# Optimization experiments

Measured on AMD Instinct MI355X. Metric: run time of the kernel, lower is better.

Reference implementation:

```python
import jax, jax.numpy as jnp
import numpy as np

N_STORE, N_DEPT, F_IN = 100_000, 20_000, 128
E = 1_000_000
H, C = 4, 16  # heads, per-head channels; hidden = H*C = 64
NUM_LAYERS = 3


def setup_inputs() -> dict:
    key = jax.random.key(0)
    ks = jax.random.split(key, 16)
    def edges(k, n_src, n_dst):
        k1, k2 = jax.random.split(k)
        src = jax.random.randint(k1, (E,), 0, n_src, dtype=jnp.int32)
        dst = jax.random.randint(k2, (E,), 0, n_dst, dtype=jnp.int32)
        return jnp.stack([src, dst])
    s = 0.05
    return {
        "x_store": jax.random.normal(ks[0], (N_STORE, F_IN), jnp.float32),
        "x_dept": jax.random.normal(ks[1], (N_DEPT, F_IN), jnp.float32),
        "edge_sd": edges(ks[2], N_STORE, N_DEPT),   # store -> dept
        "edge_ds": edges(ks[3], N_DEPT, N_STORE),   # dept  -> store
        "edge_ss": edges(ks[4], N_STORE, N_STORE),  # store -> store
        "W_src0": jax.random.normal(ks[5], (3, F_IN, H * C), jnp.float32) * s,
        "W_dst0": jax.random.normal(ks[6], (3, F_IN, H * C), jnp.float32) * s,
        "W_src_h": jax.random.normal(ks[7], (2, 3, H * C, H * C), jnp.float32) * s,
        "W_dst_h": jax.random.normal(ks[8], (2, 3, H * C, H * C), jnp.float32) * s,
        "att_src": jax.random.normal(ks[9], (3, 3, H, C), jnp.float32) * s,
        "att_dst": jax.random.normal(ks[10], (3, 3, H, C), jnp.float32) * s,
        "bias": jnp.zeros((3, 3, H * C), jnp.float32),
    }


def gat_conv(x_src, x_dst, edge, W_s, W_d, a_s, a_d, b, n_dst):
    """PyG GATConv, bipartite, add_self_loops=False, eval mode (no dropout)."""
    h_s = (x_src @ W_s).reshape(-1, H, C)   # [N_src, H, C]
    h_d = (x_dst @ W_d).reshape(-1, H, C)   # [N_dst, H, C]
    al_s = jnp.sum(h_s * a_s, axis=-1)      # [N_src, H]
    al_d = jnp.sum(h_d * a_d, axis=-1)      # [N_dst, H]
    src, dst = edge[0], edge[1]
    e = jax.nn.leaky_relu(al_s[src] + al_d[dst], 0.2)        # [E, H]
    m = jax.ops.segment_max(e, dst, num_segments=n_dst)       # segment softmax
    m = jnp.where(jnp.isfinite(m), m, 0.0)
    ex = jnp.exp(e - m[dst])
    denom = jax.ops.segment_sum(ex, dst, num_segments=n_dst)
    alpha = ex / (denom[dst] + 1e-16)                          # [E, H]
    msg = h_s[src] * alpha[:, :, None]                         # [E, H, C]
    out = jax.ops.segment_sum(msg, dst, num_segments=n_dst)    # [N_dst, H, C]
    return out.reshape(n_dst, H * C) + b


def _forward(x_store, x_dept, edge_sd, edge_ds, edge_ss,
             W_src0, W_dst0, W_src_h, W_dst_h, att_src, att_dst, bias):
    xs, xd = x_store, x_dept
    for i in range(NUM_LAYERS):
        Ws = W_src0 if i == 0 else W_src_h[i - 1]
        Wd = W_dst0 if i == 0 else W_dst_h[i - 1]
        # edge type 0: store->dept ; 1: dept->store ; 2: store->store
        o_dept = gat_conv(xs, xd, edge_sd, Ws[0], Wd[0], att_src[i, 0], att_dst[i, 0], bias[i, 0], N_DEPT)
        o1 = gat_conv(xd, xs, edge_ds, Ws[1], Wd[1], att_src[i, 1], att_dst[i, 1], bias[i, 1], N_STORE)
        o2 = gat_conv(xs, xs, edge_ss, Ws[2], Wd[2], att_src[i, 2], att_dst[i, 2], bias[i, 2], N_STORE)
        o_store = (o1 + o2) * 0.5  # HeteroConv aggr='mean' across relations into 'store'
        if i < NUM_LAYERS - 1:
            xs, xd = jax.nn.relu(o_store), jax.nn.relu(o_dept)  # dropout is identity in eval
        else:
            xs, xd = o_store, o_dept
    return jnp.concatenate([xs, xd], axis=0)  # [N_STORE + N_DEPT, 64]


def reference(x_store, x_dept, edge_sd, edge_ds, edge_ss,
              W_src0, W_dst0, W_src_h, W_dst_h, att_src, att_dst, bias):
    return _forward(x_store, x_dept, edge_sd, edge_ds, edge_ss,
                    W_src0, W_dst0, W_src_h, W_dst_h, att_src, att_dst, bias)
```

## Files before the change

### kernel.cpp

```cpp
#include <hip/hip_runtime.h>
#include <hip/hip_bf16.h>

#define N_STORE 100000
#define N_DEPT  20000
#define F_IN    128
#define NTOT    (N_DEPT + 2 * N_STORE)

#define NB0   157
#define NB12  196
#define NBUCK (NB0 + 2 * NB12)

using u16    = unsigned short;
using bf16x8 = __attribute__((ext_vector_type(8))) __bf16;
using f32x4  = __attribute__((ext_vector_type(4))) float;

__device__ __forceinline__ float b2f(u16 x) {
    unsigned u = ((unsigned)x) << 16;
    return __builtin_bit_cast(float, u);
}
__device__ __forceinline__ u16 f2b(float f) {
    unsigned u = __builtin_bit_cast(unsigned, f);
    u += 0x7FFFu + ((u >> 16) & 1u);
    return (u16)(u >> 16);
}

__global__ void k_zeroi(int* p, int n) {
    int i = blockIdx.x * 256 + threadIdx.x;
    if (i < n) p[i] = 0;
}

__global__ void k_bcount(const int* __restrict__ e0, const int* __restrict__ e1,
                         const int* __restrict__ e2, int E, int* __restrict__ bucketCnt) {
    __shared__ int c[256];
    int t = threadIdx.x;
    c[t] = 0; __syncthreads();
    int rel = blockIdx.y;
    const int* e = (rel == 0) ? e0 : (rel == 1) ? e1 : e2;
    int n = (rel == 0) ? N_DEPT : N_STORE;
    int shift = (rel == 0) ? 7 : 9;
    int i0 = blockIdx.x * 2048 + t;
#pragma unroll
    for (int k = 0; k < 8; ++k) {
        int i = i0 + k * 256;
        if (i < E) {
            int d = e[E + i];
            if ((unsigned)d < (unsigned)n) atomicAdd(&c[d >> shift], 1);
        }
    }
    __syncthreads();
    int bbase = (rel == 0) ? 0 : (rel == 1) ? NB0 : NB0 + NB12;
    int nb = (rel == 0) ? NB0 : NB12;
    if (t < nb && c[t]) atomicAdd(&bucketCnt[bbase + t], c[t]);
}

__global__ void k_bscan(const int* __restrict__ bucketCnt, int* __restrict__ bucketOfs,
                        int* __restrict__ bucketCur, int* __restrict__ offs) {
    __shared__ int s[1024];
    int t = threadIdx.x;
    int v = (t < NBUCK) ? bucketCnt[t] : 0;
    s[t] = v; __syncthreads();
    for (int o = 1; o < 1024; o <<= 1) {
        int u = (t >= o) ? s[t - o] : 0;
        __syncthreads();
        s[t] += u;
        __syncthreads();
    }
    if (t < NBUCK) {
        bucketOfs[t + 1] = s[t];
        bucketCur[t] = s[t] - v;
    }
    if (t == 0) bucketOfs[0] = 0;
    if (t == NBUCK - 1) offs[NTOT] = s[t];
}

__global__ void k_bscatter(const int* __restrict__ e0, const int* __restrict__ e1,
                           const int* __restrict__ e2, int E,
                           int* __restrict__ bucketCur, unsigned* __restrict__ pairs) {
    __shared__ int c[256];
    __shared__ int base[256];
    int t = threadIdx.x;
    c[t] = 0; __syncthreads();
    int rel = blockIdx.y;
    const int* e = (rel == 0) ? e0 : (rel == 1) ? e1 : e2;
    int n = (rel == 0) ? N_DEPT : N_STORE;
    int shift = (rel == 0) ? 7 : 9;
    int i0 = blockIdx.x * 2048 + t;
    int mb[8], mr[8]; unsigned mv[8];
#pragma unroll
    for (int k = 0; k < 8; ++k) {
        int i = i0 + k * 256;
        mb[k] = -1;
        if (i < E) {
            int d = e[E + i];
            if ((unsigned)d < (unsigned)n) {
                int b = d >> shift;
                mb[k] = b;
                mr[k] = atomicAdd(&c[b], 1);
                mv[k] = (unsigned)e[i] | ((unsigned)(d - (b << shift)) << 20);
            }
        }
    }
    __syncthreads();
    int bbase = (rel == 0) ? 0 : (rel == 1) ? NB0 : NB0 + NB12;
    int nb = (rel == 0) ? NB0 : NB12;
    if (t < nb && c[t]) base[t] = atomicAdd(&bucketCur[bbase + t], c[t]);
    __syncthreads();
#pragma unroll
    for (int k = 0; k < 8; ++k)
        if (mb[k] >= 0) pairs[base[mb[k]] + mr[k]] = mv[k];
}

__global__ void k_bfinal(const unsigned* __restrict__ pairs, const int* __restrict__ bucketOfs,
                         int* __restrict__ offs, int* __restrict__ srcs_all) {
    int b = blockIdx.x, t = threadIdx.x;
    int rel = (b < NB0) ? 0 : (b < NB0 + NB12) ? 1 : 2;
    int shift = (rel == 0) ? 7 : 9;
    int bLocal = b - ((rel == 0) ? 0 : (rel == 1) ? NB0 : NB0 + NB12);
    int n = (rel == 0) ? N_DEPT : N_STORE;
    int gbase = (rel == 0) ? 0 : (rel == 1) ? N_DEPT : N_DEPT + N_STORE;
    int nodeLo = bLocal << shift;
    int bsize = 1 << shift;
    int nNodes = n - nodeLo; if (nNodes > bsize) nNodes = bsize;
    int pairLo = bucketOfs[b], pairHi = bucketOfs[b + 1];
    __shared__ int cnt[512], sc[512];
    cnt[t] = 0; cnt[t + 256] = 0;
    __syncthreads();
    for (int p = pairLo + t; p < pairHi; p += 256)
        atomicAdd(&cnt[pairs[p] >> 20], 1);
    __syncthreads();
    sc[t] = cnt[t]; sc[t + 256] = cnt[t + 256];
    __syncthreads();
    for (int o = 1; o < 512; o <<= 1) {
        int a0 = (t >= o) ? sc[t - o] : 0;
        int a1 = (t + 256 >= o) ? sc[t + 256 - o] : 0;
        __syncthreads();
        sc[t] += a0; sc[t + 256] += a1;
        __syncthreads();
    }
    int ex0 = sc[t] - cnt[t];
    int ex1 = sc[t + 256] - cnt[t + 256];
    if (t < nNodes)       offs[gbase + nodeLo + t]       = pairLo + ex0;
    if (t + 256 < nNodes) offs[gbase + nodeLo + t + 256] = pairLo + ex1;
    __syncthreads();
    cnt[t] = ex0; cnt[t + 256] = ex1;
    __syncthreads();
    for (int p = pairLo + t; p < pairHi; p += 256) {
        unsigned u = pairs[p];
        int q = atomicAdd(&cnt[u >> 20], 1);
        srcs_all[pairLo + q] = (int)(u & 0xFFFFFu);
    }
}

__global__ void k_pack_store(const float* __restrict__ Wa, const float* __restrict__ Wb,
                             const float* __restrict__ Wd1, const float* __restrict__ Wd2,
                             const float* __restrict__ aS0, const float* __restrict__ aS2,
                             const float* __restrict__ aD1, const float* __restrict__ aD2,
                             int K, u16* __restrict__ out) {
    int id = blockIdx.x * 256 + threadIdx.x;
    int total = K * 144;
    if (id >= total) return;
    int k = id / 144, n = id - k * 144;
    float val;
    if (n < 64) val = Wa[k * 64 + n];
    else if (n < 128) val = Wb[k * 64 + (n - 64)];
    else {
        int g = (n - 128) >> 2, h = (n - 128) & 3;
        const float* W = (g == 0) ? Wa : (g == 1) ? Wb : (g == 2) ? Wd1 : Wd2;
        const float* a = (g == 0) ? aS0 : (g == 1) ? aS2 : (g == 2) ? aD1 : aD2;
        float acc = 0.f;
        for (int c = 0; c < 16; ++c) acc += W[k * 64 + h * 16 + c] * a[h * 16 + c];
        val = acc;
    }
    int KT = K >> 5;
    int ct = n >> 4, col = n & 15, kt = k >> 5, q = (k >> 3) & 3, j = k & 7;
    out[(size_t)((ct * KT + kt) * 64 + q * 16 + col) * 8 + j] = f2b(val);
}

__global__ void k_pack_dept(const float* __restrict__ Ws1, const float* __restrict__ Wd0,
                            const float* __restrict__ aD0, const float* __restrict__ aS1,
                            int K, u16* __restrict__ out) {
    int id = blockIdx.x * 256 + threadIdx.x;
    int total = K * 80;
    if (id >= total) return;
    int k = id / 80, n = id - k * 80;
    float val;
    if (n < 64) val = Ws1[k * 64 + n];
    else if (n < 72) {
        int g = (n - 64) >> 2, h = (n - 64) & 3;
        const float* W = g ? Ws1 : Wd0;
        const float* a = g ? aS1 : aD0;
        float acc = 0.f;
        for (int c = 0; c < 16; ++c) acc += W[k * 64 + h * 16 + c] * a[h * 16 + c];
        val = acc;
    } else val = 0.f;
    int KT = K >> 5;
    int ct = n >> 4, col = n & 15, kt = k >> 5, q = (k >> 3) & 3, j = k & 7;
    out[(size_t)((ct * KT + kt) * 64 + q * 16 + col) * 8 + j] = f2b(val);
}

template <int KT, int CVT>
__global__ void k_gemm(const void* __restrict__ Ain, int nrows, int K,
                       const u16* __restrict__ Bpanel, int CT,
                       u16* __restrict__ C, int cstride) {
    int wid = (blockIdx.x * blockDim.x + threadIdx.x) >> 6;
    int lane = threadIdx.x & 63;
    int m0 = wid << 4;
    if (m0 >= nrows) return;
    int r = lane & 15, q = lane >> 4;
    bf16x8 a[KT];
    if (CVT) {
        const float* ap = (const float*)Ain + (size_t)(m0 + r) * K + q * 8;
#pragma unroll
        for (int kt = 0; kt < KT; ++kt) {
            f32x4 f0 = *(const f32x4*)(ap + kt * 32);
            f32x4 f1 = *(const f32x4*)(ap + kt * 32 + 4);
            bf16x8 v;
#pragma unroll
            for (int j = 0; j < 4; ++j) {
                v[j]     = __builtin_bit_cast(__bf16, f2b(f0[j]));
                v[4 + j] = __builtin_bit_cast(__bf16, f2b(f1[j]));
            }
            a[kt] = v;
        }
    } else {
        const u16* ap = (const u16*)Ain + (size_t)(m0 + r) * K + q * 8;
#pragma unroll
        for (int kt = 0; kt < KT; ++kt) a[kt] = *(const bf16x8*)(ap + kt * 32);
    }
    const bf16x8* B = (const bf16x8*)Bpanel;
    for (int ct = 0; ct < CT; ++ct) {
        f32x4 acc = {0.f, 0.f, 0.f, 0.f};
#pragma unroll
        for (int kt = 0; kt < KT; ++kt)
            acc = __builtin_amdgcn_mfma_f32_16x16x32_bf16(a[kt], B[(ct * KT + kt) * 64 + lane], acc, 0, 0, 0);
        u16* cp = C + (size_t)m0 * cstride + ct * 16 + r;
#pragma unroll
        for (int i = 0; i < 4; ++i) cp[(size_t)(q * 4 + i) * cstride] = f2b(acc[i]);
    }
}

__device__ __forceinline__ float warp16_sum(float v) {
    v += __shfl_xor(v, 1);
    v += __shfl_xor(v, 2);
    v += __shfl_xor(v, 4);
    v += __shfl_xor(v, 8);
    return v;
}

template <int UB>
__device__ __forceinline__ void agg_seg(const int* __restrict__ srcs, int j0, int j1, int nsrc,
                                        const u16* __restrict__ tab, int stride, int hsOff, int alsOff,
                                        int lane, int slot, int h, int pbase, float ald,
                                        float& acc, float& den) {
    for (int j = j0; j < j1; j += 16) {
        int nb = j1 - j; if (nb > 16) nb = 16;
        int sv = srcs[j + (slot < nb ? slot : 0)];
        sv = ((unsigned)sv < (unsigned)nsrc) ? sv : 0;
        float av = b2f(tab[(size_t)sv * stride + alsOff + h]);
        float e = av + ald;
        e = (e > 0.f) ? e : 0.2f * e;
        float ex = (slot < nb) ? __expf(e) : 0.f;
        den += ex;
        int exi = __builtin_bit_cast(int, ex);
        for (int jj = 0; jj < nb; ) {
            int m = nb - jj; if (m > UB) m = UB;
            float exk[UB], hvk[UB];
#pragma unroll
            for (int k = 0; k < UB; ++k) {
                int idx = jj + (k < m ? k : 0);
                int s = __builtin_amdgcn_readlane(sv, idx);
                exk[k] = __builtin_bit_cast(float,
                         __builtin_amdgcn_ds_bpermute(pbase + (idx << 2), exi));
                hvk[k] = b2f(tab[(size_t)s * stride + hsOff + lane]);
            }
#pragma unroll
            for (int k = 0; k < UB; ++k)
                if (k < m) acc = fmaf(exk[k], hvk[k], acc);
            jj += m;
        }
    }
}

__global__ void k_agg1(const int* __restrict__ offs, const int* __restrict__ srcs, int ndst,
                       int nsrcmax,
                       const u16* __restrict__ srcTab, int sstride, int hsOff, int alsOff,
                       const u16* __restrict__ dstTab, int dstride, int aldOff,
                       const float* __restrict__ bias, int doRelu,
                       u16* __restrict__ bOut, float* __restrict__ fOut) {
    int wid = (blockIdx.x * blockDim.x + threadIdx.x) >> 6;
    if (wid >= ndst) return;
    int lane = threadIdx.x & 63, slot = lane & 15, h = lane >> 4;
    int pbase = (lane & 48) << 2;
    float ald = b2f(dstTab[(size_t)wid * dstride + aldOff + h]);
    int j0 = __builtin_amdgcn_readfirstlane(offs[wid]);
    int j1 = __builtin_amdgcn_readfirstlane(offs[wid + 1]);
    float acc = 0.f, den = 0.f;
    agg_seg<8>(srcs, j0, j1, nsrcmax, srcTab, sstride, hsOff, alsOff,
               lane, slot, h, pbase, ald, acc, den);
    den = warp16_sum(den);
    float out = acc / (den + 1e-16f) + bias[lane];
    if (doRelu) out = out > 0.f ? out : 0.f;
    size_t oi = (size_t)wid * 64 + lane;
    if (fOut) fOut[oi] = out;
    else      bOut[oi] = f2b(out);
}

__global__ void k_agg2(const int* __restrict__ offs1, const int* __restrict__ srcs,
                       const int* __restrict__ offs2,
                       const u16* __restrict__ projD, const u16* __restrict__ projS,
                       const float* __restrict__ bias1, const float* __restrict__ bias2,
                       int doRelu,
                       u16* __restrict__ bOut, float* __restrict__ fOut) {
    int wid = (blockIdx.x * blockDim.x + threadIdx.x) >> 6;
    if (wid >= N_STORE) return;
    int lane = threadIdx.x & 63, slot = lane & 15, h = lane >> 4;
    int pbase = (lane & 48) << 2;
    const u16* myrow = projS + (size_t)wid * 144;
    float ald1 = b2f(myrow[136 + h]);
    float ald2 = b2f(myrow[140 + h]);
    int a0 = __builtin_amdgcn_readfirstlane(offs1[wid]);
    int a1e = __builtin_amdgcn_readfirstlane(offs1[wid + 1]);
    int b0 = __builtin_amdgcn_readfirstlane(offs2[wid]);
    int b1e = __builtin_amdgcn_readfirstlane(offs2[wid + 1]);
    float acc1 = 0.f, den1 = 0.f, acc2 = 0.f, den2 = 0.f;
    agg_seg<8>(srcs, a0, a1e, N_DEPT, projD, 80, 0, 68,
               lane, slot, h, pbase, ald1, acc1, den1);
    agg_seg<8>(srcs, b0, b1e, N_STORE, projS, 144, 64, 132,
               lane, slot, h, pbase, ald2, acc2, den2);
    den1 = warp16_sum(den1);
    den2 = warp16_sum(den2);
    float out = (acc1 / (den1 + 1e-16f) + bias1[lane] + acc2 / (den2 + 1e-16f) + bias2[lane]) * 0.5f;
    if (doRelu) out = out > 0.f ? out : 0.f;
    size_t oi = (size_t)wid * 64 + lane;
    if (fOut) fOut[oi] = out;
    else      bOut[oi] = f2b(out);
}

extern "C" void kernel_launch(void* const* d_in, const int* in_sizes, int n_in,
                              void* d_out, int out_size, void* d_ws, size_t ws_size,
                              hipStream_t stream) {
    const float* x_store = (const float*)d_in[0];
    const float* x_dept  = (const float*)d_in[1];
    const int* e_sd = (const int*)d_in[2];
    const int* e_ds = (const int*)d_in[3];
    const int* e_ss = (const int*)d_in[4];
    const float* W_src0  = (const float*)d_in[5];
    const float* W_dst0  = (const float*)d_in[6];
    const float* W_src_h = (const float*)d_in[7];
    const float* W_dst_h = (const float*)d_in[8];
    const float* att_src = (const float*)d_in[9];
    const float* att_dst = (const float*)d_in[10];
    const float* bias    = (const float*)d_in[11];
    const int E = in_sizes[2] / 2;

    char* w = (char*)d_ws;
    auto alloc = [&](size_t bytes) -> char* {
        char* p = w;
        w += (bytes + 255) & ~(size_t)255;
        return p;
    };
    int* offs_all  = (int*)alloc((size_t)(NTOT + 1) * 4);
    int* srcs_all  = (int*)alloc((size_t)3 * E * 4);
    int* bucketCnt = (int*)alloc(1024 * 4);
    int* bucketOfs = (int*)alloc(1024 * 4);
    int* bucketCur = (int*)alloc(1024 * 4);
    u16* panelS[3]; u16* panelD[3];
    for (int l = 0; l < 3; ++l) {
        int KT = (l == 0) ? 4 : 2;
        panelS[l] = (u16*)alloc((size_t)KT * 9 * 64 * 8 * 2);
        panelD[l] = (u16*)alloc((size_t)KT * 5 * 64 * 8 * 2);
    }
    u16* projS  = (u16*)alloc((size_t)N_STORE * 144 * 2);
    u16* projD  = (u16*)alloc((size_t)N_DEPT * 80 * 2);
    u16* actSA  = (u16*)alloc((size_t)N_STORE * 64 * 2);
    u16* actDA  = (u16*)alloc((size_t)N_DEPT * 64 * 2);
    u16* actSB  = actSA;
    u16* actDB  = actDA;
    unsigned* pairs = (unsigned*)projS;

    int* off_sd = offs_all;
    int* off_ds = offs_all + N_DEPT;
    int* off_ss = offs_all + N_DEPT + N_STORE;

    float* outStoreF = (float*)d_out;
    float* outDeptF  = outStoreF + (size_t)N_STORE * 64;

    int ebl8 = (E + 2047) / 2048;
    k_zeroi<<<(NBUCK + 255) / 256, 256, 0, stream>>>(bucketCnt, NBUCK);
    k_bcount<<<dim3(ebl8, 3), 256, 0, stream>>>(e_sd, e_ds, e_ss, E, bucketCnt);
    k_bscan<<<1, 1024, 0, stream>>>(bucketCnt, bucketOfs, bucketCur, offs_all);
    k_bscatter<<<dim3(ebl8, 3), 256, 0, stream>>>(e_sd, e_ds, e_ss, E, bucketCur, pairs);
    k_bfinal<<<NBUCK, 256, 0, stream>>>(pairs, bucketOfs, offs_all, srcs_all);

    for (int l = 0; l < 3; ++l) {
        int K = (l == 0) ? 128 : 64;
        const float *Ws[3], *Wd[3], *aS[3], *aD[3];
        for (int rr = 0; rr < 3; ++rr) {
            Ws[rr] = (l == 0) ? W_src0 + (size_t)rr * 128 * 64
                              : W_src_h + (size_t)((l - 1) * 3 + rr) * 64 * 64;
            Wd[rr] = (l == 0) ? W_dst0 + (size_t)rr * 128 * 64
                              : W_dst_h + (size_t)((l - 1) * 3 + rr) * 64 * 64;
            aS[rr] = att_src + (size_t)(l * 3 + rr) * 64;
            aD[rr] = att_dst + (size_t)(l * 3 + rr) * 64;
        }
        k_pack_store<<<(K * 144 + 255) / 256, 256, 0, stream>>>(
            Ws[0], Ws[2], Wd[1], Wd[2], aS[0], aS[2], aD[1], aD[2], K, panelS[l]);
        k_pack_dept<<<(K * 80 + 255) / 256, 256, 0, stream>>>(
            Ws[1], Wd[0], aD[0], aS[1], K, panelD[l]);

        int gbS = (N_STORE / 16 * 64 + 255) / 256;
        int gbD = (N_DEPT / 16 * 64 + 255) / 256;
        if (l == 0) {
            k_gemm<4, 1><<<gbS, 256, 0, stream>>>(x_store, N_STORE, K, panelS[l], 9, projS, 144);
            k_gemm<4, 1><<<gbD, 256, 0, stream>>>(x_dept, N_DEPT, K, panelD[l], 5, projD, 80);
        } else if (l == 1) {
            k_gemm<2, 0><<<gbS, 256, 0, stream>>>(actSA, N_STORE, K, panelS[l], 9, projS, 144);
            k_gemm<2, 0><<<gbD, 256, 0, stream>>>(actDA, N_DEPT, K, panelD[l], 5, projD, 80);
        } else {
            k_gemm<2, 0><<<gbS, 256, 0, stream>>>(actSB, N_STORE, K, panelS[l], 9, projS, 144);
            k_gemm<2, 0><<<gbD, 256, 0, stream>>>(actDB, N_DEPT, K, panelD[l], 5, projD, 80);
        }

        int relu = (l < 2) ? 1 : 0;
        u16* bS = (l == 0) ? actSA : actSB;
        u16* bD = (l == 0) ? actDA : actDB;
        float* fS = (l == 2) ? outStoreF : nullptr;
        float* fD = (l == 2) ? outDeptF  : nullptr;
        k_agg1<<<N_DEPT / 4, 256, 0, stream>>>(
            off_sd, srcs_all, N_DEPT, N_STORE,
            projS, 144, 0, 128,
            projD, 80, 64,
            bias + (size_t)(l * 3 + 0) * 64, relu, bD, fD);
        k_agg2<<<N_STORE / 4, 256, 0, stream>>>(
            off_ds, srcs_all, off_ss,
            projD, projS,
            bias + (size_t)(l * 3 + 1) * 64, bias + (size_t)(l * 3 + 2) * 64,
            relu, bS, fS);
    }
    (void)n_in; (void)out_size; (void)ws_size;
}
```

Baseline: 680.9 us.

## Split projection tables into aligned 64-wide arrays and batch sixteen gathers

The GEMM epilogue now writes each projected feature block into its own 64-column bf16 table and the attention logits into a separate 16-column table, instead of one wide interleaved 144- or 80-column row. This makes every gathered source row a contiguous, aligned 128-byte read. The aggregation loop issues all 16 neighbour-row gathers up front for each chunk, rather than in sub-batches of up to 8, to expose more memory-level parallelism. The cost is redundant loads and bpermutes on partial chunks, which matters for low-degree store segments, plus higher register pressure from the 16-wide unroll.

```diff
diff --git a/kernel.cpp b/kernel.cpp
--- a/kernel.cpp
+++ b/kernel.cpp
@@ -198,10 +198,11 @@
     out[(size_t)((ct * KT + kt) * 64 + q * 16 + col) * 8 + j] = f2b(val);
 }
 
-template <int KT, int CVT>
+template <int KT, int CVT, int MODE>
 __global__ void k_gemm(const void* __restrict__ Ain, int nrows, int K,
-                       const u16* __restrict__ Bpanel, int CT,
-                       u16* __restrict__ C, int cstride) {
+                       const u16* __restrict__ Bpanel,
+                       u16* __restrict__ H0, u16* __restrict__ H1, u16* __restrict__ AL) {
+    const int CT = (MODE == 0) ? 9 : 5;
     int wid = (blockIdx.x * blockDim.x + threadIdx.x) >> 6;
     int lane = threadIdx.x & 63;
     int m0 = wid << 4;
@@ -228,14 +229,38 @@
         for (int kt = 0; kt < KT; ++kt) a[kt] = *(const bf16x8*)(ap + kt * 32);
     }
     const bf16x8* B = (const bf16x8*)Bpanel;
+    int rowb = m0 + q * 4;
+#pragma unroll
     for (int ct = 0; ct < CT; ++ct) {
         f32x4 acc = {0.f, 0.f, 0.f, 0.f};
 #pragma unroll
         for (int kt = 0; kt < KT; ++kt)
             acc = __builtin_amdgcn_mfma_f32_16x16x32_bf16(a[kt], B[(ct * KT + kt) * 64 + lane], acc, 0, 0, 0);
-        u16* cp = C + (size_t)m0 * cstride + ct * 16 + r;
-#pragma unroll
-        for (int i = 0; i < 4; ++i) cp[(size_t)(q * 4 + i) * cstride] = f2b(acc[i]);
+        if (MODE == 0) {
+            if (ct < 4) {
+                u16* cp = H0 + (size_t)rowb * 64 + ct * 16 + r;
+#pragma unroll
+                for (int i = 0; i < 4; ++i) cp[(size_t)i * 64] = f2b(acc[i]);
+            } else if (ct < 8) {
+                u16* cp = H1 + (size_t)rowb * 64 + (ct - 4) * 16 + r;
+#pragma unroll
+                for (int i = 0; i < 4; ++i) cp[(size_t)i * 64] = f2b(acc[i]);
+            } else {
+                u16* cp = AL + (size_t)rowb * 16 + r;
+#pragma unroll
+                for (int i = 0; i < 4; ++i) cp[(size_t)i * 16] = f2b(acc[i]);
+            }
+        } else {
+            if (ct < 4) {
+                u16* cp = H0 + (size_t)rowb * 64 + ct * 16 + r;
+#pragma unroll
+                for (int i = 0; i < 4; ++i) cp[(size_t)i * 64] = f2b(acc[i]);
+            } else {
+                u16* cp = AL + (size_t)rowb * 16 + r;
+#pragma unroll
+                for (int i = 0; i < 4; ++i) cp[(size_t)i * 16] = f2b(acc[i]);
+            }
+        }
     }
 }
 
@@ -247,56 +272,49 @@
     return v;
 }
 
-template <int UB>
 __device__ __forceinline__ void agg_seg(const int* __restrict__ srcs, int j0, int j1, int nsrc,
-                                        const u16* __restrict__ tab, int stride, int hsOff, int alsOff,
-                                        int lane, int slot, int h, int pbase, float ald,
+                                        const u16* __restrict__ htab, const u16* __restrict__ altab,
+                                        int alsOff, int lane, int slot, int h, int pbase, float ald,
                                         float& acc, float& den) {
     for (int j = j0; j < j1; j += 16) {
         int nb = j1 - j; if (nb > 16) nb = 16;
         int sv = srcs[j + (slot < nb ? slot : 0)];
         sv = ((unsigned)sv < (unsigned)nsrc) ? sv : 0;
-        float av = b2f(tab[(size_t)sv * stride + alsOff + h]);
-        float e = av + ald;
+        u16 avr = altab[(size_t)sv * 16 + alsOff + h];
+        float hv[16];
+#pragma unroll
+        for (int k = 0; k < 16; ++k) {
+            int s = __builtin_amdgcn_readlane(sv, k);
+            hv[k] = b2f(htab[(size_t)s * 64 + lane]);
+        }
+        float e = b2f(avr) + ald;
         e = (e > 0.f) ? e : 0.2f * e;
         float ex = (slot < nb) ? __expf(e) : 0.f;
         den += ex;
         int exi = __builtin_bit_cast(int, ex);
-        for (int jj = 0; jj < nb; ) {
-            int m = nb - jj; if (m > UB) m = UB;
-            float exk[UB], hvk[UB];
-#pragma unroll
-            for (int k = 0; k < UB; ++k) {
-                int idx = jj + (k < m ? k : 0);
-                int s = __builtin_amdgcn_readlane(sv, idx);
-                exk[k] = __builtin_bit_cast(float,
-                         __builtin_amdgcn_ds_bpermute(pbase + (idx << 2), exi));
-                hvk[k] = b2f(tab[(size_t)s * stride + hsOff + lane]);
-            }
-#pragma unroll
-            for (int k = 0; k < UB; ++k)
-                if (k < m) acc = fmaf(exk[k], hvk[k], acc);
-            jj += m;
-        }
-    }
-}
-
-__global__ void k_agg1(const int* __restrict__ offs, const int* __restrict__ srcs, int ndst,
-                       int nsrcmax,
-                       const u16* __restrict__ srcTab, int sstride, int hsOff, int alsOff,
-                       const u16* __restrict__ dstTab, int dstride, int aldOff,
+#pragma unroll
+        for (int k = 0; k < 16; ++k) {
+            float exv = __builtin_bit_cast(float,
+                __builtin_amdgcn_ds_bpermute(pbase + (k << 2), exi));
+            acc = fmaf(exv, hv[k], acc);
+        }
+    }
+}
+
+__global__ void k_agg1(const int* __restrict__ offs, const int* __restrict__ srcs,
+                       const u16* __restrict__ hS0, const u16* __restrict__ alS,
+                       const u16* __restrict__ alD,
                        const float* __restrict__ bias, int doRelu,
                        u16* __restrict__ bOut, float* __restrict__ fOut) {
     int wid = (blockIdx.x * blockDim.x + threadIdx.x) >> 6;
-    if (wid >= ndst) return;
+    if (wid >= N_DEPT) return;
     int lane = threadIdx.x & 63, slot = lane & 15, h = lane >> 4;
     int pbase = (lane & 48) << 2;
-    float ald = b2f(dstTab[(size_t)wid * dstride + aldOff + h]);
+    float ald = b2f(alD[(size_t)wid * 16 + 0 + h]);
     int j0 = __builtin_amdgcn_readfirstlane(offs[wid]);
     int j1 = __builtin_amdgcn_readfirstlane(offs[wid + 1]);
     float acc = 0.f, den = 0.f;
-    agg_seg<8>(srcs, j0, j1, nsrcmax, srcTab, sstride, hsOff, alsOff,
-               lane, slot, h, pbase, ald, acc, den);
+    agg_seg(srcs, j0, j1, N_STORE, hS0, alS, 0, lane, slot, h, pbase, ald, acc, den);
     den = warp16_sum(den);
     float out = acc / (den + 1e-16f) + bias[lane];
     if (doRelu) out = out > 0.f ? out : 0.f;
@@ -307,7 +325,8 @@
 
 __global__ void k_agg2(const int* __restrict__ offs1, const int* __restrict__ srcs,
                        const int* __restrict__ offs2,
-                       const u16* __restrict__ projD, const u16* __restrict__ projS,
+                       const u16* __restrict__ hD, const u16* __restrict__ alD,
+                       const u16* __restrict__ hS2, const u16* __restrict__ alS,
                        const float* __restrict__ bias1, const float* __restrict__ bias2,
                        int doRelu,
                        u16* __restrict__ bOut, float* __restrict__ fOut) {
@@ -315,18 +334,15 @@
     if (wid >= N_STORE) return;
     int lane = threadIdx.x & 63, slot = lane & 15, h = lane >> 4;
     int pbase = (lane & 48) << 2;
-    const u16* myrow = projS + (size_t)wid * 144;
-    float ald1 = b2f(myrow[136 + h]);
-    float ald2 = b2f(myrow[140 + h]);
+    float ald1 = b2f(alS[(size_t)wid * 16 + 8 + h]);
+    float ald2 = b2f(alS[(size_t)wid * 16 + 12 + h]);
     int a0 = __builtin_amdgcn_readfirstlane(offs1[wid]);
     int a1e = __builtin_amdgcn_readfirstlane(offs1[wid + 1]);
     int b0 = __builtin_amdgcn_readfirstlane(offs2[wid]);
     int b1e = __builtin_amdgcn_readfirstlane(offs2[wid + 1]);
     float acc1 = 0.f, den1 = 0.f, acc2 = 0.f, den2 = 0.f;
-    agg_seg<8>(srcs, a0, a1e, N_DEPT, projD, 80, 0, 68,
-               lane, slot, h, pbase, ald1, acc1, den1);
-    agg_seg<8>(srcs, b0, b1e, N_STORE, projS, 144, 64, 132,
-               lane, slot, h, pbase, ald2, acc2, den2);
+    agg_seg(srcs, a0, a1e, N_DEPT, hD, alD, 4, lane, slot, h, pbase, ald1, acc1, den1);
+    agg_seg(srcs, b0, b1e, N_STORE, hS2, alS, 4, lane, slot, h, pbase, ald2, acc2, den2);
     den1 = warp16_sum(den1);
     den2 = warp16_sum(den2);
     float out = (acc1 / (den1 + 1e-16f) + bias1[lane] + acc2 / (den2 + 1e-16f) + bias2[lane]) * 0.5f;
@@ -370,13 +386,16 @@
         panelS[l] = (u16*)alloc((size_t)KT * 9 * 64 * 8 * 2);
         panelD[l] = (u16*)alloc((size_t)KT * 5 * 64 * 8 * 2);
     }
-    u16* projS  = (u16*)alloc((size_t)N_STORE * 144 * 2);
-    u16* projD  = (u16*)alloc((size_t)N_DEPT * 80 * 2);
-    u16* actSA  = (u16*)alloc((size_t)N_STORE * 64 * 2);
-    u16* actDA  = (u16*)alloc((size_t)N_DEPT * 64 * 2);
-    u16* actSB  = actSA;
-    u16* actDB  = actDA;
-    unsigned* pairs = (unsigned*)projS;
+    u16* hS0   = (u16*)alloc((size_t)N_STORE * 64 * 2);
+    u16* hS2   = (u16*)alloc((size_t)N_STORE * 64 * 2);
+    u16* alS   = (u16*)alloc((size_t)N_STORE * 16 * 2);
+    u16* hD    = (u16*)alloc((size_t)N_DEPT * 64 * 2);
+    u16* alD   = (u16*)alloc((size_t)N_DEPT * 16 * 2);
+    u16* actSA = (u16*)alloc((size_t)N_STORE * 64 * 2);
+    u16* actDA = (u16*)alloc((size_t)N_DEPT * 64 * 2);
+    u16* actSB = actSA;
+    u16* actDB = actDA;
+    unsigned* pairs = (unsigned*)hS0;
 
     int* off_sd = offs_all;
     int* off_ds = offs_all + N_DEPT;
@@ -411,14 +430,14 @@
         int gbS = (N_STORE / 16 * 64 + 255) / 256;
         int gbD = (N_DEPT / 16 * 64 + 255) / 256;
         if (l == 0) {
-            k_gemm<4, 1><<<gbS, 256, 0, stream>>>(x_store, N_STORE, K, panelS[l], 9, projS, 144);
-            k_gemm<4, 1><<<gbD, 256, 0, stream>>>(x_dept, N_DEPT, K, panelD[l], 5, projD, 80);
+            k_gemm<4, 1, 0><<<gbS, 256, 0, stream>>>(x_store, N_STORE, K, panelS[l], hS0, hS2, alS);
+            k_gemm<4, 1, 1><<<gbD, 256, 0, stream>>>(x_dept, N_DEPT, K, panelD[l], hD, nullptr, alD);
         } else if (l == 1) {
-            k_gemm<2, 0><<<gbS, 256, 0, stream>>>(actSA, N_STORE, K, panelS[l], 9, projS, 144);
-            k_gemm<2, 0><<<gbD, 256, 0, stream>>>(actDA, N_DEPT, K, panelD[l], 5, projD, 80);
+            k_gemm<2, 0, 0><<<gbS, 256, 0, stream>>>(actSA, N_STORE, K, panelS[l], hS0, hS2, alS);
+            k_gemm<2, 0, 1><<<gbD, 256, 0, stream>>>(actDA, N_DEPT, K, panelD[l], hD, nullptr, alD);
         } else {
-            k_gemm<2, 0><<<gbS, 256, 0, stream>>>(actSB, N_STORE, K, panelS[l], 9, projS, 144);
-            k_gemm<2, 0><<<gbD, 256, 0, stream>>>(actDB, N_DEPT, K, panelD[l], 5, projD, 80);
+            k_gemm<2, 0, 0><<<gbS, 256, 0, stream>>>(actSB, N_STORE, K, panelS[l], hS0, hS2, alS);
+            k_gemm<2, 0, 1><<<gbD, 256, 0, stream>>>(actDB, N_DEPT, K, panelD[l], hD, nullptr, alD);
         }
 
         int relu = (l < 2) ? 1 : 0;
@@ -427,13 +446,11 @@
         float* fS = (l == 2) ? outStoreF : nullptr;
         float* fD = (l == 2) ? outDeptF  : nullptr;
         k_agg1<<<N_DEPT / 4, 256, 0, stream>>>(
-            off_sd, srcs_all, N_DEPT, N_STORE,
-            projS, 144, 0, 128,
-            projD, 80, 64,
+            off_sd, srcs_all, hS0, alS, alD,
             bias + (size_t)(l * 3 + 0) * 64, relu, bD, fD);
         k_agg2<<<N_STORE / 4, 256, 0, stream>>>(
             off_ds, srcs_all, off_ss,
-            projD, projS,
+            hD, alD, hS2, alS,
             bias + (size_t)(l * 3 + 1) * 64, bias + (size_t)(l * 3 + 2) * 64,
             relu, bS, fS);
     }
```

After: 578.5 us. -15.0%, faster.
